# Kernel optimization log

Measured on AMD Instinct MI355X. Metric: run time of the kernel, lower is better.

The kernel has to match this reference:

```python
import jax, jax.numpy as jnp
import numpy as np

C = 512

def _conv1x1(x, w, b):
    # x: [B, C, T], w: [O, C], b: [O] -> [B, O, T]
    return jnp.einsum('oc,bct->bot', w, x) + b[None, :, None]

def setup_inputs() -> dict:
    key = jax.random.key(0)
    ks = jax.random.split(key, 9)
    B, T = 8, 2048
    s = 1.0 / np.sqrt(C)
    inp = {'x': jax.random.normal(ks[0], (B, C, T), dtype=jnp.float32)}
    names = ['theta', 'phi', 'g', 'w']
    for i, n in enumerate(names):
        inp[f'w_{n}'] = jax.random.uniform(ks[1 + 2 * i], (C, C), jnp.float32, -s, s)
        inp[f'b_{n}'] = jax.random.uniform(ks[2 + 2 * i], (C,), jnp.float32, -s, s)
    return inp

def reference(x, w_theta, b_theta, w_phi, b_phi, w_g, b_g, w_w, b_w):
    relu = jax.nn.relu
    feat_theta = relu(_conv1x1(x, w_theta, b_theta))          # [B, C, T]
    feat_phi = relu(_conv1x1(x, w_phi, b_phi))                # [B, C, T]
    # scores: Q^T K over channel dim -> [B, T, T]
    scores = jnp.einsum('bci,bcj->bij', feat_theta, feat_phi)
    attn = jax.nn.softmax(scores, axis=2)                     # [B, T, T]
    feat_g = relu(_conv1x1(x, w_g, b_g))                      # [B, C, T]
    # attention-weighted V: [B, T, T] x [B, T, C] -> [B, T, C] -> [B, C, T]
    feature = jnp.einsum('bij,bcj->bci', attn, feat_g)
    w_feature = relu(_conv1x1(feature, w_w, b_w))
    return w_feature + x
```

## Files before the change

kernel.cpp:

```cpp
#include <hip/hip_runtime.h>
#include <math.h>

#define C_DIM 512
#define T_DIM 2048
#define B_DIM 8

typedef _Float16 f16;
typedef __attribute__((ext_vector_type(8))) _Float16 half8;
typedef __attribute__((ext_vector_type(4))) _Float16 half4;
typedef __attribute__((ext_vector_type(4))) float floatx4;

__global__ __launch_bounds__(256) void convert_w_kernel(
    const float* __restrict__ w0, const float* __restrict__ w1,
    const float* __restrict__ w2, const float* __restrict__ w3,
    f16* __restrict__ o0, f16* __restrict__ o1,
    f16* __restrict__ o2, f16* __restrict__ o3)
{
    const float* src; f16* dst;
    switch (blockIdx.z) {
        case 0:  src = w0; dst = o0; break;
        case 1:  src = w1; dst = o1; break;
        case 2:  src = w2; dst = o2; break;
        default: src = w3; dst = o3; break;
    }
    const int idx = (blockIdx.x * 256 + threadIdx.x) * 4;
    const float4 v = *(const float4*)(src + idx);
    half4 h; h[0] = (f16)v.x; h[1] = (f16)v.y; h[2] = (f16)v.z; h[3] = (f16)v.w;
    *(half4*)(dst + idx) = h;
}

__global__ __launch_bounds__(256) void concat_bias_kernel(
    const float* __restrict__ b0, const float* __restrict__ b1,
    float* __restrict__ o)
{
    const int i = blockIdx.x * 256 + threadIdx.x;
    o[i] = (i < 512) ? b0[i] : b1[i - 512];
}

__global__ __launch_bounds__(256) void transpose_x_kernel(
    const float* __restrict__ x, f16* __restrict__ xt)
{
    __shared__ float xs[32][33];
    const int b  = blockIdx.z;
    const int t0 = blockIdx.x * 32, c0 = blockIdx.y * 32;
    const float* xb = x + (size_t)b * C_DIM * T_DIM;
    const int r = threadIdx.x >> 3, q = threadIdx.x & 7;

    const float4 v = *(const float4*)(xb + (size_t)(c0 + r) * T_DIM + t0 + q * 4);
    xs[r][q * 4 + 0] = v.x; xs[r][q * 4 + 1] = v.y;
    xs[r][q * 4 + 2] = v.z; xs[r][q * 4 + 3] = v.w;
    __syncthreads();

    f16* xtb = xt + (size_t)b * C_DIM * T_DIM;
    half4 h;
    h[0] = (f16)xs[q * 4 + 0][r]; h[1] = (f16)xs[q * 4 + 1][r];
    h[2] = (f16)xs[q * 4 + 2][r]; h[3] = (f16)xs[q * 4 + 3][r];
    *(half4*)(xtb + (size_t)(t0 + r) * C_DIM + c0 + q * 4) = h;
}

template<int MODE>
__global__ __launch_bounds__(256) void gemm_tn(
    const f16* __restrict__ A, size_t sA, int lda,
    const f16* __restrict__ B, size_t sB, int ldb,
    void* __restrict__ Cp, size_t sC, int ldc,
    const float* __restrict__ bias,
    const float* __restrict__ resid, size_t sR,
    int K)
{
    __shared__ __align__(16) f16 As[2][128 * 32];
    __shared__ __align__(16) f16 Bs[2][128 * 32];

    const int gx = gridDim.x;
    const int flat = blockIdx.y * gx + blockIdx.x;
    const int jsc = gx >> 2;
    const int sh = (jsc <= 1) ? 0 : (31 - __builtin_clz(jsc));
    const int s = flat >> 4, rem = flat & 15;
    const int i0 = ((s >> sh) * 4 + (rem >> 2)) * 128;
    const int j0 = (((jsc <= 1) ? 0 : (s & (jsc - 1))) * 4 + (rem & 3)) * 128;

    const int bz = blockIdx.z;
    A += (size_t)bz * sA;
    B += (size_t)bz * sB;

    const int tid  = threadIdx.x;
    const int lane = tid & 63;
    const int wave = tid >> 6;
    const int wy = wave >> 1, wx = wave & 1;
    const int quad = lane >> 4, l16 = lane & 15;

    const int row1 = tid >> 2, ch = tid & 3;
    const int row2 = row1 + 64;
    const int w1 = row1 * 32 + ((ch ^ (row1 & 3)) << 3);
    const int w2 = row2 * 32 + ((ch ^ (row2 & 3)) << 3);

    const f16* gA1 = A + (size_t)(i0 + row1) * lda + ch * 8;
    const f16* gA2 = A + (size_t)(i0 + row2) * lda + ch * 8;
    const f16* gB1 = B + (size_t)(j0 + row1) * ldb + ch * 8;
    const f16* gB2 = B + (size_t)(j0 + row2) * ldb + ch * 8;

    const int xa = (quad ^ (l16 & 3)) << 3;

    const int nt = K >> 5;

    float4 a1_0 = *(const float4*)(gA1);      float4 a2_0 = *(const float4*)(gA2);
    float4 b1_0 = *(const float4*)(gB1);      float4 b2_0 = *(const float4*)(gB2);
    float4 a1_1 = *(const float4*)(gA1 + 32); float4 a2_1 = *(const float4*)(gA2 + 32);
    float4 b1_1 = *(const float4*)(gB1 + 32); float4 b2_1 = *(const float4*)(gB2 + 32);

    floatx4 acc[4][4] = {};

    for (int t = 0; t < nt; t += 2) {
        *(float4*)&As[0][w1] = a1_0;
        *(float4*)&As[0][w2] = a2_0;
        *(float4*)&Bs[0][w1] = b1_0;
        *(float4*)&Bs[0][w2] = b2_0;
        if (t + 2 < nt) {
            const int off = (t + 2) * 32;
            a1_0 = *(const float4*)(gA1 + off); a2_0 = *(const float4*)(gA2 + off);
            b1_0 = *(const float4*)(gB1 + off); b2_0 = *(const float4*)(gB2 + off);
        }
        __syncthreads();
        {
            half8 af[4], bf[4];
            #pragma unroll
            for (int mi = 0; mi < 4; ++mi)
                af[mi] = *(const half8*)&As[0][(wy * 64 + mi * 16 + l16) * 32 + xa];
            #pragma unroll
            for (int ni = 0; ni < 4; ++ni)
                bf[ni] = *(const half8*)&Bs[0][(wx * 64 + ni * 16 + l16) * 32 + xa];
            #pragma unroll
            for (int mi = 0; mi < 4; ++mi)
                #pragma unroll
                for (int ni = 0; ni < 4; ++ni)
                    acc[mi][ni] = __builtin_amdgcn_mfma_f32_16x16x32_f16(
                        af[mi], bf[ni], acc[mi][ni], 0, 0, 0);
        }
        *(float4*)&As[1][w1] = a1_1;
        *(float4*)&As[1][w2] = a2_1;
        *(float4*)&Bs[1][w1] = b1_1;
        *(float4*)&Bs[1][w2] = b2_1;
        if (t + 3 < nt) {
            const int off = (t + 3) * 32;
            a1_1 = *(const float4*)(gA1 + off); a2_1 = *(const float4*)(gA2 + off);
            b1_1 = *(const float4*)(gB1 + off); b2_1 = *(const float4*)(gB2 + off);
        }
        __syncthreads();
        {
            half8 af[4], bf[4];
            #pragma unroll
            for (int mi = 0; mi < 4; ++mi)
                af[mi] = *(const half8*)&As[1][(wy * 64 + mi * 16 + l16) * 32 + xa];
            #pragma unroll
            for (int ni = 0; ni < 4; ++ni)
                bf[ni] = *(const half8*)&Bs[1][(wx * 64 + ni * 16 + l16) * 32 + xa];
            #pragma unroll
            for (int mi = 0; mi < 4; ++mi)
                #pragma unroll
                for (int ni = 0; ni < 4; ++ni)
                    acc[mi][ni] = __builtin_amdgcn_mfma_f32_16x16x32_f16(
                        af[mi], bf[ni], acc[mi][ni], 0, 0, 0);
        }
    }

    #pragma unroll
    for (int mi = 0; mi < 4; ++mi) {
        #pragma unroll
        for (int ni = 0; ni < 4; ++ni) {
            const int col = j0 + wx * 64 + ni * 16 + l16;
            #pragma unroll
            for (int r = 0; r < 4; ++r) {
                const int row = i0 + wy * 64 + mi * 16 + quad * 4 + r;
                float v = acc[mi][ni][r];
                if (MODE == 1) { v += bias[col]; v = v > 0.f ? v : 0.f; }
                if (MODE == 2) { v += bias[row]; v = v > 0.f ? v : 0.f; }
                if (MODE == 3) {
                    v += bias[row];
                    v = v > 0.f ? v : 0.f;
                    v += resid[(size_t)bz * sR + (size_t)row * ldc + col];
                    ((float*)Cp)[(size_t)bz * sC + (size_t)row * ldc + col] = v;
                } else {
                    ((f16*)Cp)[(size_t)bz * sC + (size_t)row * ldc + col] = (f16)v;
                }
            }
        }
    }
}

__global__ __launch_bounds__(256) void softmax_f16_kernel(f16* __restrict__ S)
{
    f16* p = S + (size_t)blockIdx.x * T_DIM;
    const int tid = threadIdx.x;

    half8 hv = *((const half8*)p + tid);
    float v[8];
    float lmax = -1e30f;
    #pragma unroll
    for (int c = 0; c < 8; ++c) { v[c] = (float)hv[c]; lmax = fmaxf(lmax, v[c]); }
    #pragma unroll
    for (int off = 32; off; off >>= 1)
        lmax = fmaxf(lmax, __shfl_down(lmax, off));
    __shared__ float redm[4];
    if ((tid & 63) == 0) redm[tid >> 6] = lmax;
    __syncthreads();
    const float m = fmaxf(fmaxf(redm[0], redm[1]), fmaxf(redm[2], redm[3]));

    float lsum = 0.f;
    #pragma unroll
    for (int c = 0; c < 8; ++c) { v[c] = __expf(v[c] - m); lsum += v[c]; }
    #pragma unroll
    for (int off = 32; off; off >>= 1)
        lsum += __shfl_down(lsum, off);
    __shared__ float reds[4];
    if ((tid & 63) == 0) reds[tid >> 6] = lsum;
    __syncthreads();
    const float inv = 1.f / (reds[0] + reds[1] + reds[2] + reds[3]);

    #pragma unroll
    for (int c = 0; c < 8; ++c) hv[c] = (f16)(v[c] * inv);
    *((half8*)p + tid) = hv;
}

extern "C" void kernel_launch(void* const* d_in, const int* in_sizes, int n_in,
                              void* d_out, int out_size, void* d_ws, size_t ws_size,
                              hipStream_t stream)
{
    const float* x       = (const float*)d_in[0];
    const float* w_theta = (const float*)d_in[1];
    const float* b_theta = (const float*)d_in[2];
    const float* w_phi   = (const float*)d_in[3];
    const float* b_phi   = (const float*)d_in[4];
    const float* w_g     = (const float*)d_in[5];
    const float* b_g     = (const float*)d_in[6];
    const float* w_w     = (const float*)d_in[7];
    const float* b_w     = (const float*)d_in[8];
    float* out = (float*)d_out;

    const size_t FE = (size_t)B_DIM * C_DIM * T_DIM;
    const size_t TC = (size_t)T_DIM * C_DIM;
    const size_t TT = (size_t)T_DIM * T_DIM;

    f16* xt      = (f16*)d_ws;
    f16* wtp     = xt + FE;
    f16* wg_h    = wtp + 524288;
    f16* ww_h    = wg_h + 262144;
    float* btp   = (float*)(ww_h + 262144);
    f16* tp      = (f16*)(btp + 1024);
    f16* g       = tp + (size_t)B_DIM * T_DIM * 1024;
    f16* scores  = g + FE;
    f16* feature = tp;

    const dim3 blk(256);

    convert_w_kernel<<<dim3(256, 1, 4), blk, 0, stream>>>(
        w_theta, w_phi, w_g, w_w, wtp, wtp + 262144, wg_h, ww_h);
    concat_bias_kernel<<<dim3(4), blk, 0, stream>>>(b_theta, b_phi, btp);
    transpose_x_kernel<<<dim3(T_DIM / 32, C_DIM / 32, B_DIM), blk, 0, stream>>>(x, xt);

    gemm_tn<1><<<dim3(1024 / 128, T_DIM / 128, B_DIM), blk, 0, stream>>>(
        xt, TC, C_DIM, wtp, 0, C_DIM, tp, (size_t)T_DIM * 1024, 1024,
        btp, nullptr, 0, C_DIM);
    gemm_tn<2><<<dim3(T_DIM / 128, C_DIM / 128, B_DIM), blk, 0, stream>>>(
        wg_h, 0, C_DIM, xt, TC, C_DIM, g, TC, T_DIM, b_g, nullptr, 0, C_DIM);
    gemm_tn<0><<<dim3(T_DIM / 128, T_DIM / 128, B_DIM), blk, 0, stream>>>(
        tp, (size_t)T_DIM * 1024, 1024, tp + 512, (size_t)T_DIM * 1024, 1024,
        scores, TT, T_DIM, nullptr, nullptr, 0, C_DIM);
    softmax_f16_kernel<<<dim3(B_DIM * T_DIM), blk, 0, stream>>>(scores);
    gemm_tn<0><<<dim3(C_DIM / 128, T_DIM / 128, B_DIM), blk, 0, stream>>>(
        scores, TT, T_DIM, g, TC, T_DIM, feature, TC, C_DIM, nullptr, nullptr, 0, T_DIM);
    gemm_tn<3><<<dim3(T_DIM / 128, C_DIM / 128, B_DIM), blk, 0, stream>>>(
        ww_h, 0, C_DIM, feature, TC, C_DIM, out, TC, T_DIM, b_w, x, TC, C_DIM);
}
```

Baseline: 268.2 us.

## Add 256x256-tile double-buffered GEMM for theta/phi projection and score GEMMs

Introduces a new 512-thread GEMM kernel with 256x256 output tiles, LDS double buffering and register prefetch of the next K-slices. Each wave computes a 128x64 sub-tile using 16x16x32 f16 MFMA, with s_setprio raised around the MFMA bursts. The kernel is used for the fused theta/phi projection and for the scores GEMM, replacing the 128x128 generic kernel. The goal is more data reuse per LDS load and better overlap of global loads with MFMA work. In exchange it needs heavy register use (128 accumulator floats per thread) and launches fewer blocks, which may lower occupancy.

```diff
diff --git a/kernel.cpp b/kernel.cpp
--- a/kernel.cpp
+++ b/kernel.cpp
@@ -186,6 +186,143 @@
     }
 }
 
+template<int MODE>
+__global__ __launch_bounds__(512, 2) void gemm256(
+    const f16* __restrict__ A, size_t sA, int lda,
+    const f16* __restrict__ B, size_t sB, int ldb,
+    void* __restrict__ Cp, size_t sC, int ldc,
+    const float* __restrict__ bias,
+    int K)
+{
+    __shared__ __align__(16) f16 As[2][256 * 32];
+    __shared__ __align__(16) f16 Bs[2][256 * 32];
+
+    const int i0 = blockIdx.y * 256;
+    const int j0 = blockIdx.x * 256;
+    const int bz = blockIdx.z;
+    A += (size_t)bz * sA;
+    B += (size_t)bz * sB;
+
+    const int tid  = threadIdx.x;
+    const int lane = tid & 63;
+    const int wave = tid >> 6;
+    const int wy = wave >> 2;
+    const int wx = wave & 3;
+    const int quad = lane >> 4, l16 = lane & 15;
+
+    const int srow = tid >> 2, sch = tid & 3;
+    const f16* gA0 = A + (size_t)(i0 + srow) * lda + sch * 8;
+    const f16* gA1 = A + (size_t)(i0 + 128 + srow) * lda + sch * 8;
+    const f16* gB0 = B + (size_t)(j0 + srow) * ldb + sch * 8;
+    const f16* gB1 = B + (size_t)(j0 + 128 + srow) * ldb + sch * 8;
+    const int w0 = srow * 32 + sch * 8;
+    const int w1 = w0 + 128 * 32;
+
+    const int ra = (wy * 128 + l16) * 32 + quad * 8;
+    const int rb = (wx * 64 + l16) * 32 + quad * 8;
+
+    const int nt = K >> 5;
+
+    float4 a0_0 = *(const float4*)(gA0);      float4 a1_0 = *(const float4*)(gA1);
+    float4 b0_0 = *(const float4*)(gB0);      float4 b1_0 = *(const float4*)(gB1);
+    float4 a0_1 = *(const float4*)(gA0 + 32); float4 a1_1 = *(const float4*)(gA1 + 32);
+    float4 b0_1 = *(const float4*)(gB0 + 32); float4 b1_1 = *(const float4*)(gB1 + 32);
+
+    floatx4 acc[8][4] = {};
+
+    for (int t = 0; t < nt; t += 2) {
+        *(float4*)&As[0][w0] = a0_0; *(float4*)&As[0][w1] = a1_0;
+        *(float4*)&Bs[0][w0] = b0_0; *(float4*)&Bs[0][w1] = b1_0;
+        if (t + 2 < nt) {
+            const int off = (t + 2) * 32;
+            a0_0 = *(const float4*)(gA0 + off); a1_0 = *(const float4*)(gA1 + off);
+            b0_0 = *(const float4*)(gB0 + off); b1_0 = *(const float4*)(gB1 + off);
+        }
+        asm volatile("s_waitcnt lgkmcnt(0)\ns_barrier" ::: "memory");
+        {
+            half8 af[4], bf[4];
+            #pragma unroll
+            for (int ni = 0; ni < 4; ++ni)
+                bf[ni] = *(const half8*)&Bs[0][rb + ni * 512];
+            #pragma unroll
+            for (int mi = 0; mi < 4; ++mi)
+                af[mi] = *(const half8*)&As[0][ra + mi * 512];
+            __builtin_amdgcn_s_setprio(1);
+            #pragma unroll
+            for (int mi = 0; mi < 4; ++mi)
+                #pragma unroll
+                for (int ni = 0; ni < 4; ++ni)
+                    acc[mi][ni] = __builtin_amdgcn_mfma_f32_16x16x32_f16(
+                        af[mi], bf[ni], acc[mi][ni], 0, 0, 0);
+            __builtin_amdgcn_s_setprio(0);
+            asm volatile("s_barrier" ::: "memory");
+            #pragma unroll
+            for (int mi = 0; mi < 4; ++mi)
+                af[mi] = *(const half8*)&As[0][ra + 2048 + mi * 512];
+            __builtin_amdgcn_s_setprio(1);
+            #pragma unroll
+            for (int mi = 0; mi < 4; ++mi)
+                #pragma unroll
+                for (int ni = 0; ni < 4; ++ni)
+                    acc[4 + mi][ni] = __builtin_amdgcn_mfma_f32_16x16x32_f16(
+                        af[mi], bf[ni], acc[4 + mi][ni], 0, 0, 0);
+            __builtin_amdgcn_s_setprio(0);
+        }
+        *(float4*)&As[1][w0] = a0_1; *(float4*)&As[1][w1] = a1_1;
+        *(float4*)&Bs[1][w0] = b0_1; *(float4*)&Bs[1][w1] = b1_1;
+        if (t + 3 < nt) {
+            const int off = (t + 3) * 32;
+            a0_1 = *(const float4*)(gA0 + off); a1_1 = *(const float4*)(gA1 + off);
+            b0_1 = *(const float4*)(gB0 + off); b1_1 = *(const float4*)(gB1 + off);
+        }
+        asm volatile("s_waitcnt lgkmcnt(0)\ns_barrier" ::: "memory");
+        {
+            half8 af[4], bf[4];
+            #pragma unroll
+            for (int ni = 0; ni < 4; ++ni)
+                bf[ni] = *(const half8*)&Bs[1][rb + ni * 512];
+            #pragma unroll
+            for (int mi = 0; mi < 4; ++mi)
+                af[mi] = *(const half8*)&As[1][ra + mi * 512];
+            __builtin_amdgcn_s_setprio(1);
+            #pragma unroll
+            for (int mi = 0; mi < 4; ++mi)
+                #pragma unroll
+                for (int ni = 0; ni < 4; ++ni)
+                    acc[mi][ni] = __builtin_amdgcn_mfma_f32_16x16x32_f16(
+                        af[mi], bf[ni], acc[mi][ni], 0, 0, 0);
+            __builtin_amdgcn_s_setprio(0);
+            asm volatile("s_barrier" ::: "memory");
+            #pragma unroll
+            for (int mi = 0; mi < 4; ++mi)
+                af[mi] = *(const half8*)&As[1][ra + 2048 + mi * 512];
+            __builtin_amdgcn_s_setprio(1);
+            #pragma unroll
+            for (int mi = 0; mi < 4; ++mi)
+                #pragma unroll
+                for (int ni = 0; ni < 4; ++ni)
+                    acc[4 + mi][ni] = __builtin_amdgcn_mfma_f32_16x16x32_f16(
+                        af[mi], bf[ni], acc[4 + mi][ni], 0, 0, 0);
+            __builtin_amdgcn_s_setprio(0);
+        }
+    }
+
+    #pragma unroll
+    for (int m = 0; m < 8; ++m) {
+        #pragma unroll
+        for (int ni = 0; ni < 4; ++ni) {
+            const int col = j0 + wx * 64 + ni * 16 + l16;
+            #pragma unroll
+            for (int r = 0; r < 4; ++r) {
+                const int row = i0 + wy * 128 + m * 16 + quad * 4 + r;
+                float v = acc[m][ni][r];
+                if (MODE == 1) { v += bias[col]; v = v > 0.f ? v : 0.f; }
+                ((f16*)Cp)[(size_t)bz * sC + (size_t)row * ldc + col] = (f16)v;
+            }
+        }
+    }
+}
+
 __global__ __launch_bounds__(256) void softmax_f16_kernel(f16* __restrict__ S)
 {
     f16* p = S + (size_t)blockIdx.x * T_DIM;
@@ -250,20 +387,21 @@
     f16* feature = tp;
 
     const dim3 blk(256);
+    const dim3 blk512(512);
 
     convert_w_kernel<<<dim3(256, 1, 4), blk, 0, stream>>>(
         w_theta, w_phi, w_g, w_w, wtp, wtp + 262144, wg_h, ww_h);
     concat_bias_kernel<<<dim3(4), blk, 0, stream>>>(b_theta, b_phi, btp);
     transpose_x_kernel<<<dim3(T_DIM / 32, C_DIM / 32, B_DIM), blk, 0, stream>>>(x, xt);
 
-    gemm_tn<1><<<dim3(1024 / 128, T_DIM / 128, B_DIM), blk, 0, stream>>>(
+    gemm256<1><<<dim3(1024 / 256, T_DIM / 256, B_DIM), blk512, 0, stream>>>(
         xt, TC, C_DIM, wtp, 0, C_DIM, tp, (size_t)T_DIM * 1024, 1024,
-        btp, nullptr, 0, C_DIM);
+        btp, C_DIM);
     gemm_tn<2><<<dim3(T_DIM / 128, C_DIM / 128, B_DIM), blk, 0, stream>>>(
         wg_h, 0, C_DIM, xt, TC, C_DIM, g, TC, T_DIM, b_g, nullptr, 0, C_DIM);
-    gemm_tn<0><<<dim3(T_DIM / 128, T_DIM / 128, B_DIM), blk, 0, stream>>>(
+    gemm256<0><<<dim3(T_DIM / 256, T_DIM / 256, B_DIM), blk512, 0, stream>>>(
         tp, (size_t)T_DIM * 1024, 1024, tp + 512, (size_t)T_DIM * 1024, 1024,
-        scores, TT, T_DIM, nullptr, nullptr, 0, C_DIM);
+        scores, TT, T_DIM, nullptr, C_DIM);
     softmax_f16_kernel<<<dim3(B_DIM * T_DIM), blk, 0, stream>>>(scores);
     gemm_tn<0><<<dim3(C_DIM / 128, T_DIM / 128, B_DIM), blk, 0, stream>>>(
         scores, TT, T_DIM, g, TC, T_DIM, feature, TC, C_DIM, nullptr, nullptr, 0, T_DIM);
```

Result: no change. 268.9 us (+0.2%).

## Add 256x256-tile GEMM with direct global-to-LDS loads for theta/phi and scores

Applied to the files above, without the earlier changes.

Introduces a 512-thread GEMM kernel with 256x256 output tiles, double-buffered LDS filled through global_load_lds, raised wave priority around MFMA bursts, and a grouped block-index swizzle for L2 locality. It replaces the 128-tile GEMM for the fused theta/phi projection and for the T×T score computation, aiming to raise data reuse per load and cut instruction overhead for staging. The larger tile uses many accumulator registers and needs 2 blocks per CU, which risks spilling or low occupancy, and the block count shrinks for the smaller projection GEMM.

```diff
diff --git a/kernel.cpp b/kernel.cpp
--- a/kernel.cpp
+++ b/kernel.cpp
@@ -186,6 +186,132 @@
     }
 }
 
+__device__ __forceinline__ void gl16(const f16* g, f16* l)
+{
+    __builtin_amdgcn_global_load_lds(
+        (const __attribute__((address_space(1))) unsigned int*)g,
+        (__attribute__((address_space(3))) unsigned int*)l,
+        16, 0, 0);
+}
+
+template<int MODE>
+__global__ __launch_bounds__(512, 2) void gemm256(
+    const f16* __restrict__ A, size_t sA, int lda,
+    const f16* __restrict__ B, size_t sB, int ldb,
+    void* __restrict__ Cp, size_t sC, int ldc,
+    const float* __restrict__ bias,
+    int K)
+{
+    __shared__ __align__(16) f16 As[2][256 * 32];
+    __shared__ __align__(16) f16 Bs[2][256 * 32];
+
+    const int gx = gridDim.x;
+    const int flat = blockIdx.y * gx + blockIdx.x;
+    const int jsc = gx >> 2;
+    const int sh = (jsc <= 1) ? 0 : (31 - __builtin_clz(jsc));
+    const int s = flat >> 4, rem = flat & 15;
+    const int i0 = ((s >> sh) * 4 + (rem >> 2)) * 256;
+    const int j0 = (((jsc <= 1) ? 0 : (s & (jsc - 1))) * 4 + (rem & 3)) * 256;
+
+    const int bz = blockIdx.z;
+    A += (size_t)bz * sA;
+    B += (size_t)bz * sB;
+
+    const int tid  = threadIdx.x;
+    const int lane = tid & 63;
+    const int wave = tid >> 6;
+    const int wy = wave >> 2;
+    const int wx = wave & 3;
+    const int quad = lane >> 4, l16 = lane & 15;
+
+    const int srow = wave * 32 + (lane >> 2);
+    const int sch  = lane & 3;
+    const f16* gAs0 = A + (size_t)(i0 + srow) * lda + sch * 8;
+    const f16* gAs1 = gAs0 + (size_t)16 * lda;
+    const f16* gBs0 = B + (size_t)(j0 + srow) * ldb + sch * 8;
+    const f16* gBs1 = gBs0 + (size_t)16 * ldb;
+    const int wsg = wave * 1024;
+
+    const int ra = (wy * 128 + l16) * 32 + quad * 8;
+    const int rb = (wx * 64 + l16) * 32 + quad * 8;
+
+    const int nt = K >> 5;
+
+    gl16(gAs0,      &As[0][wsg]); gl16(gAs1,      &As[0][wsg + 512]);
+    gl16(gBs0,      &Bs[0][wsg]); gl16(gBs1,      &Bs[0][wsg + 512]);
+    gl16(gAs0 + 32, &As[1][wsg]); gl16(gAs1 + 32, &As[1][wsg + 512]);
+    gl16(gBs0 + 32, &Bs[1][wsg]); gl16(gBs1 + 32, &Bs[1][wsg + 512]);
+
+    floatx4 acc[8][4] = {};
+
+#define MFMA8(M0, AF0, AF1)                                                   \
+    do {                                                                      \
+        __builtin_amdgcn_s_setprio(1);                                        \
+        _Pragma("unroll")                                                     \
+        for (int ni = 0; ni < 4; ++ni)                                        \
+            acc[M0][ni] = __builtin_amdgcn_mfma_f32_16x16x32_f16(             \
+                AF0, bf[ni], acc[M0][ni], 0, 0, 0);                           \
+        _Pragma("unroll")                                                     \
+        for (int ni = 0; ni < 4; ++ni)                                        \
+            acc[(M0) + 1][ni] = __builtin_amdgcn_mfma_f32_16x16x32_f16(       \
+                AF1, bf[ni], acc[(M0) + 1][ni], 0, 0, 0);                     \
+        __builtin_amdgcn_s_setprio(0);                                        \
+    } while (0)
+
+    for (int t = 0; t < nt; ++t) {
+        if (t < nt - 1)
+            asm volatile("s_waitcnt vmcnt(4)\ns_barrier" ::: "memory");
+        else
+            asm volatile("s_waitcnt vmcnt(0)\ns_barrier" ::: "memory");
+
+        const f16* sa = &As[t & 1][0];
+        const f16* sb = &Bs[t & 1][0];
+
+        half8 bf[4];
+        #pragma unroll
+        for (int ni = 0; ni < 4; ++ni)
+            bf[ni] = *(const half8*)&sb[rb + ni * 512];
+
+        half8 af0 = *(const half8*)&sa[ra];
+        half8 af1 = *(const half8*)&sa[ra + 512];
+        MFMA8(0, af0, af1);
+        af0 = *(const half8*)&sa[ra + 1024];
+        af1 = *(const half8*)&sa[ra + 1536];
+        MFMA8(2, af0, af1);
+        af0 = *(const half8*)&sa[ra + 2048];
+        af1 = *(const half8*)&sa[ra + 2560];
+        MFMA8(4, af0, af1);
+        af0 = *(const half8*)&sa[ra + 3072];
+        af1 = *(const half8*)&sa[ra + 3584];
+        MFMA8(6, af0, af1);
+
+        asm volatile("s_barrier" ::: "memory");
+        if (t + 2 < nt) {
+            const int off = (t + 2) * 32;
+            f16* stA = &As[t & 1][wsg];
+            f16* stB = &Bs[t & 1][wsg];
+            gl16(gAs0 + off, stA); gl16(gAs1 + off, stA + 512);
+            gl16(gBs0 + off, stB); gl16(gBs1 + off, stB + 512);
+        }
+    }
+#undef MFMA8
+
+    #pragma unroll
+    for (int m = 0; m < 8; ++m) {
+        #pragma unroll
+        for (int ni = 0; ni < 4; ++ni) {
+            const int col = j0 + wx * 64 + ni * 16 + l16;
+            #pragma unroll
+            for (int r = 0; r < 4; ++r) {
+                const int row = i0 + wy * 128 + m * 16 + quad * 4 + r;
+                float v = acc[m][ni][r];
+                if (MODE == 1) { v += bias[col]; v = v > 0.f ? v : 0.f; }
+                ((f16*)Cp)[(size_t)bz * sC + (size_t)row * ldc + col] = (f16)v;
+            }
+        }
+    }
+}
+
 __global__ __launch_bounds__(256) void softmax_f16_kernel(f16* __restrict__ S)
 {
     f16* p = S + (size_t)blockIdx.x * T_DIM;
@@ -250,20 +376,21 @@
     f16* feature = tp;
 
     const dim3 blk(256);
+    const dim3 blk512(512);
 
     convert_w_kernel<<<dim3(256, 1, 4), blk, 0, stream>>>(
         w_theta, w_phi, w_g, w_w, wtp, wtp + 262144, wg_h, ww_h);
     concat_bias_kernel<<<dim3(4), blk, 0, stream>>>(b_theta, b_phi, btp);
     transpose_x_kernel<<<dim3(T_DIM / 32, C_DIM / 32, B_DIM), blk, 0, stream>>>(x, xt);
 
-    gemm_tn<1><<<dim3(1024 / 128, T_DIM / 128, B_DIM), blk, 0, stream>>>(
+    gemm256<1><<<dim3(1024 / 256, T_DIM / 256, B_DIM), blk512, 0, stream>>>(
         xt, TC, C_DIM, wtp, 0, C_DIM, tp, (size_t)T_DIM * 1024, 1024,
-        btp, nullptr, 0, C_DIM);
+        btp, C_DIM);
     gemm_tn<2><<<dim3(T_DIM / 128, C_DIM / 128, B_DIM), blk, 0, stream>>>(
         wg_h, 0, C_DIM, xt, TC, C_DIM, g, TC, T_DIM, b_g, nullptr, 0, C_DIM);
-    gemm_tn<0><<<dim3(T_DIM / 128, T_DIM / 128, B_DIM), blk, 0, stream>>>(
+    gemm256<0><<<dim3(T_DIM / 256, T_DIM / 256, B_DIM), blk512, 0, stream>>>(
         tp, (size_t)T_DIM * 1024, 1024, tp + 512, (size_t)T_DIM * 1024, 1024,
-        scores, TT, T_DIM, nullptr, nullptr, 0, C_DIM);
+        scores, TT, T_DIM, nullptr, C_DIM);
     softmax_f16_kernel<<<dim3(B_DIM * T_DIM), blk, 0, stream>>>(scores);
     gemm_tn<0><<<dim3(C_DIM / 128, T_DIM / 128, B_DIM), blk, 0, stream>>>(
         scores, TT, T_DIM, g, TC, T_DIM, feature, TC, C_DIM, nullptr, nullptr, 0, T_DIM);
```

Measured after the change: 290.6 us. 8.3% more time.
